# Kernel tuning notes

Measured on AMD Instinct MI355X. Metric: run time of the kernel, lower is better.

## Reference

```python
import jax, jax.numpy as jnp
import numpy as np

N, E, D, HGC, LG, NC = 20000, 320000, 256, 256, 4, 2
BN_EPS = 1e-5


def setup_inputs() -> dict:
    key = jax.random.key(0)
    ks = jax.random.split(key, 12)
    features = jax.random.normal(ks[0], (N, D), jnp.float32)
    edge_index = jax.random.randint(ks[1], (2, E), 0, N)
    edgenet_input = jax.random.uniform(ks[2], (E, 6), dtype=jnp.float32)
    edge_weight_override = jax.random.uniform(ks[3], (E,), dtype=jnp.float32)
    # ChebConv weights: K=3 weight matrices per layer; layer0 in=D==HGC so one stack works
    cheb_w = jax.random.normal(ks[4], (LG, 3, HGC, HGC), jnp.float32) * np.float32((2.0 / HGC) ** 0.5)
    w1 = jax.random.normal(ks[5], (LG * HGC, 256), jnp.float32) * np.float32((2.0 / (LG * HGC)) ** 0.5)
    b1 = jnp.zeros((256,), jnp.float32)
    bn_gamma = jnp.ones((256,), jnp.float32)
    bn_beta = jnp.zeros((256,), jnp.float32)
    bn_mean = jnp.zeros((256,), jnp.float32)
    bn_var = jnp.ones((256,), jnp.float32)
    w2 = jax.random.normal(ks[6], (256, NC), jnp.float32) * np.float32((2.0 / 256.0) ** 0.5)
    b2 = jnp.zeros((NC,), jnp.float32)
    return dict(features=features, edge_index=edge_index, edgenet_input=edgenet_input,
                edge_weight_override=edge_weight_override, cheb_w=cheb_w,
                w1=w1, b1=b1, bn_gamma=bn_gamma, bn_beta=bn_beta,
                bn_mean=bn_mean, bn_var=bn_var, w2=w2, b2=b2)


def reference(features, edge_index, edgenet_input, edge_weight_override, cheb_w,
              w1, b1, bn_gamma, bn_beta, bn_mean, bn_var, w2, b2):
    # eval mode: dropout / edge_dropout are no-ops; edge_weight_override bypasses PAE
    ew = edge_weight_override  # [E]
    row, col = edge_index[0], edge_index[1]  # source, target (PyG source_to_target)
    n = features.shape[0]
    # sym-normalized scaled Laplacian, lambda_max=2: L_hat = -D^{-1/2} A D^{-1/2} (diag 1-1=0)
    deg = jax.ops.segment_sum(ew, row, num_segments=n)
    dis = jnp.where(deg > 0, jax.lax.rsqrt(deg), 0.0)
    norm = -(dis[row] * ew * dis[col])  # [E]

    def prop(x):  # out[col] += norm * x[row]
        return jax.ops.segment_sum(norm[:, None] * x[row], col, num_segments=n)

    def cheb(x, W):  # W: [3, in, out]; Chebyshev recursion T0=x, T1=L_hat x, T2=2 L_hat T1 - T0
        tx0 = x
        tx1 = prop(x)
        out = tx0 @ W[0] + tx1 @ W[1]
        tx2 = 2.0 * prop(tx1) - tx0
        return out + tx2 @ W[2]

    h = jax.nn.relu(cheb(features, cheb_w[0]))
    jk = h
    for i in range(1, cheb_w.shape[0]):
        h = jax.nn.relu(cheb(h, cheb_w[i]))
        jk = jnp.concatenate((jk, h), axis=1)
    # classifier: Linear -> ReLU -> BatchNorm1d(eval) -> Linear
    z = jax.nn.relu(jk @ w1 + b1)
    z = (z - bn_mean) * (bn_gamma * jax.lax.rsqrt(bn_var + BN_EPS)) + bn_beta
    logit = z @ w2 + b2
    return logit, ew
```

## Files before the change

### kernel.cpp

```cpp
#include <hip/hip_runtime.h>
#include <hip/hip_bf16.h>

#define NN 20000
#define EE 320000
#define LGN 4

typedef unsigned short u16;
typedef short bf16x8 __attribute__((ext_vector_type(8)));
typedef float f32x4 __attribute__((ext_vector_type(4)));

__device__ __forceinline__ float bf2f(u16 v) {
    unsigned int u = ((unsigned int)v) << 16;
    float f; __builtin_memcpy(&f, &u, 4); return f;
}
__device__ __forceinline__ u16 f2bf(float f) {
    __hip_bfloat16 h = __float2bfloat16(f);
    u16 u; __builtin_memcpy(&u, &h, 2); return u;
}

__device__ __forceinline__ void gll16(const void* g, void* l) {
    __builtin_amdgcn_global_load_lds(
        (const __attribute__((address_space(1))) unsigned int*)g,
        (__attribute__((address_space(3))) unsigned int*)l, 16, 0, 0);
}

__global__ __launch_bounds__(256) void k_edge1(const int* __restrict__ ei,
                                               const float* __restrict__ ew,
                                               float* __restrict__ deg,
                                               int* __restrict__ counts,
                                               float* __restrict__ out_ew) {
    int e = blockIdx.x * 256 + threadIdx.x;
    if (e >= EE) return;
    int r = ei[e];
    float w = ew[e];
    atomicAdd(&deg[r], w);
    atomicAdd(&counts[ei[EE + e]], 1);
    out_ew[e] = w;
}

__global__ __launch_bounds__(256) void k_rsqrt(float* __restrict__ deg) {
    int i = blockIdx.x * 256 + threadIdx.x;
    if (i >= NN) return;
    float d = deg[i];
    deg[i] = (d > 0.f) ? rsqrtf(d) : 0.f;
}

__global__ __launch_bounds__(1024) void k_scan(const int* __restrict__ counts,
                                               int* __restrict__ offs) {
    __shared__ int part[1024];
    int t = threadIdx.x;
    const int C = (NN + 1023) / 1024;
    int lo = t * C, hi = min(lo + C, NN);
    int s = 0;
    for (int i = lo; i < hi; i++) s += counts[i];
    part[t] = s;
    __syncthreads();
    for (int off = 1; off < 1024; off <<= 1) {
        int add = (t >= off) ? part[t - off] : 0;
        __syncthreads();
        part[t] += add;
        __syncthreads();
    }
    int base = part[t] - s;
    for (int i = lo; i < hi; i++) { offs[i] = base; base += counts[i]; }
    if (t == 1023) offs[NN] = part[1023];
}

__global__ __launch_bounds__(256) void k_scatter(const int* __restrict__ ei,
                                                 const float* __restrict__ ew,
                                                 const float* __restrict__ dis,
                                                 const int* __restrict__ offs,
                                                 int* __restrict__ cursor,
                                                 int2* __restrict__ nbrs) {
    int e = blockIdx.x * 256 + threadIdx.x;
    if (e >= EE) return;
    int r = ei[e], c = ei[EE + e];
    float nm = -(dis[r] * ew[e] * dis[c]);
    int pidx = offs[c] + atomicAdd(&cursor[c], 1);
    nbrs[pidx] = make_int2(r, __float_as_int(nm));
}

__global__ __launch_bounds__(256) void k_cast(const float* __restrict__ src,
                                              u16* __restrict__ dst, int n) {
    int i = blockIdx.x * 256 + threadIdx.x;
    if (i < n) dst[i] = f2bf(src[i]);
}

__global__ __launch_bounds__(256) void k_cast_T(const float* __restrict__ src,
                                                u16* __restrict__ dst, int K) {
    __shared__ u16 tile[32][33];
    int kt = blockIdx.x * 32, nt = blockIdx.y * 32;
    int tx = threadIdx.x & 31, ty = threadIdx.x >> 5;
#pragma unroll
    for (int i = 0; i < 32; i += 8)
        tile[ty + i][tx] = f2bf(src[(size_t)(kt + ty + i) * 256 + (nt + tx)]);
    __syncthreads();
#pragma unroll
    for (int i = 0; i < 32; i += 8)
        dst[(size_t)(nt + ty + i) * K + (kt + tx)] = tile[tx][ty + i];
}

__global__ __launch_bounds__(256) void k_foldbn(const float* __restrict__ g,
                                                const float* __restrict__ be,
                                                const float* __restrict__ mn,
                                                const float* __restrict__ vr,
                                                float* __restrict__ sc,
                                                float* __restrict__ sh) {
    int t = threadIdx.x;
    if (t < 256) {
        float s = g[t] * rsqrtf(vr[t] + 1e-5f);
        sc[t] = s;
        sh[t] = be[t] - mn[t] * s;
    }
}

__global__ __launch_bounds__(256) void k_prop(const u16* __restrict__ x, int ldx,
                                              const u16* __restrict__ xsub, int ldsub,
                                              int dotx2,
                                              u16* __restrict__ out, int ldo,
                                              const int* __restrict__ offs,
                                              const int2* __restrict__ nbrs) {
    int c = __builtin_amdgcn_readfirstlane(blockIdx.x * 4 + (threadIdx.x >> 6));
    int lane = threadIdx.x & 63;
    int s = offs[c], e = offs[c + 1];
    float a0 = 0.f, a1 = 0.f, a2 = 0.f, a3 = 0.f;
    for (int i = s; i < e; i += 8) {
        int2 mm[8];
        ushort4 xv[8];
#pragma unroll
        for (int j = 0; j < 8; j++) mm[j] = nbrs[i + j];
#pragma unroll
        for (int j = 0; j < 8; j++)
            xv[j] = *(const ushort4*)(x + (size_t)mm[j].x * ldx + lane * 4);
#pragma unroll
        for (int j = 0; j < 8; j++) {
            float w = (i + j < e) ? __int_as_float(mm[j].y) : 0.f;
            a0 += w * bf2f(xv[j].x);
            a1 += w * bf2f(xv[j].y);
            a2 += w * bf2f(xv[j].z);
            a3 += w * bf2f(xv[j].w);
        }
    }
    if (dotx2) {
        ushort4 xs = *(const ushort4*)(xsub + (size_t)c * ldsub + lane * 4);
        a0 = 2.f * a0 - bf2f(xs.x);
        a1 = 2.f * a1 - bf2f(xs.y);
        a2 = 2.f * a2 - bf2f(xs.z);
        a3 = 2.f * a3 - bf2f(xs.w);
    }
    ushort4 o;
    o.x = f2bf(a0); o.y = f2bf(a1); o.z = f2bf(a2); o.w = f2bf(a3);
    *(ushort4*)(out + (size_t)c * ldo + lane * 4) = o;
}

__global__ __launch_bounds__(256, 2) void k_gemm(
    const u16* __restrict__ A0, const u16* __restrict__ A1,
    const u16* __restrict__ A2, const u16* __restrict__ A3,
    int lda0, int lda1, int lda2, int lda3,
    int K, const u16* __restrict__ Bt,
    int mode,
    u16* __restrict__ outb, int ldob,
    const float* __restrict__ bias, const float* __restrict__ sc,
    const float* __restrict__ sh,
    const float* __restrict__ w2, const float* __restrict__ b2,
    float* __restrict__ outlog) {
    __shared__ __align__(16) u16 lds[2 * 20 * 512];
    int t = threadIdx.x;
    int wv = t >> 6, l = t & 63;
    int q = l >> 4, l16 = l & 15;
    int m0 = blockIdx.x * 64;
    int n0 = wv * 64;
    const int steps = K >> 5;

    f32x4 acc[4][4] = {};

    int arow = min(m0 + wv * 16 + l16, NN - 1);

    auto stage = [&](int buf, int s) {
        int kt = s * 32;
        u16* base = lds + buf * 20 * 512;
#pragma unroll
        for (int j = 0; j < 4; j++) {
            const u16* bg = Bt + (size_t)((wv * 4 + j) * 16 + l16) * K + kt + q * 8;
            gll16(bg, base + (wv * 4 + j) * 512);
        }
        int ch = kt >> 8;
        const u16* ap;
        int la;
        if (ch == 0) { ap = A0; la = lda0; }
        else if (ch == 1) { ap = A1; la = lda1; }
        else if (ch == 2) { ap = A2; la = lda2; }
        else { ap = A3; la = lda3; }
        gll16(ap + (size_t)arow * la + (kt & 255) + q * 8, base + (16 + wv) * 512);
    };

    stage(0, 0);
    for (int s = 0; s < steps; s++) {
        __syncthreads();
        if (s + 1 < steps) stage((s + 1) & 1, s + 1);
        const u16* base = lds + (s & 1) * 20 * 512;
        bf16x8 a[4], b[4];
#pragma unroll
        for (int mh = 0; mh < 4; mh++)
            a[mh] = *(const bf16x8*)(base + (16 + mh) * 512 + l * 8);
#pragma unroll
        for (int j = 0; j < 4; j++)
            b[j] = *(const bf16x8*)(base + (wv * 4 + j) * 512 + l * 8);
#pragma unroll
        for (int mh = 0; mh < 4; mh++)
#pragma unroll
            for (int j = 0; j < 4; j++)
                acc[mh][j] =
                    __builtin_amdgcn_mfma_f32_16x16x32_bf16(a[mh], b[j], acc[mh][j], 0, 0, 0);
    }
    __syncthreads();

    if (mode == 0) {
        u16* Cs = lds + wv * 4608;
#pragma unroll
        for (int mh = 0; mh < 4; mh++)
#pragma unroll
            for (int j = 0; j < 4; j++)
#pragma unroll
                for (int i = 0; i < 4; i++) {
                    float v = acc[mh][j][i];
                    v = v > 0.f ? v : 0.f;
                    Cs[(mh * 16 + q * 4 + i) * 72 + j * 16 + l16] = f2bf(v);
                }
#pragma unroll
        for (int j = 0; j < 8; j++) {
            int f = j * 64 + l;
            int r = f >> 3, cc = (f & 7) * 8;
            uint4 cv = *(const uint4*)&Cs[r * 72 + cc];
            int row = m0 + r;
            if (row < NN) *(uint4*)(outb + (size_t)row * ldob + n0 + cc) = cv;
        }
    } else {
        float bi[4], s4[4], h4[4], wa[4], wb[4];
#pragma unroll
        for (int j = 0; j < 4; j++) {
            int col = n0 + j * 16 + l16;
            bi[j] = bias[col];
            s4[j] = sc[col];
            h4[j] = sh[col];
            wa[j] = w2[2 * col];
            wb[j] = w2[2 * col + 1];
        }
        float* red = (float*)lds;
#pragma unroll
        for (int mh = 0; mh < 4; mh++)
#pragma unroll
            for (int i = 0; i < 4; i++) {
                float p0 = 0.f, p1 = 0.f;
#pragma unroll
                for (int j = 0; j < 4; j++) {
                    float v = acc[mh][j][i] + bi[j];
                    v = v > 0.f ? v : 0.f;
                    v = v * s4[j] + h4[j];
                    p0 += v * wa[j];
                    p1 += v * wb[j];
                }
#pragma unroll
                for (int off = 1; off < 16; off <<= 1) {
                    p0 += __shfl_xor(p0, off, 64);
                    p1 += __shfl_xor(p1, off, 64);
                }
                if (l16 == 0) {
                    int rl = mh * 16 + q * 4 + i;
                    red[(wv * 64 + rl) * 2 + 0] = p0;
                    red[(wv * 64 + rl) * 2 + 1] = p1;
                }
            }
        __syncthreads();
        if (t < 128) {
            int rl = t >> 1, cp = t & 1;
            float v = red[(0 * 64 + rl) * 2 + cp] + red[(1 * 64 + rl) * 2 + cp] +
                      red[(2 * 64 + rl) * 2 + cp] + red[(3 * 64 + rl) * 2 + cp];
            int row = m0 + rl;
            if (row < NN) outlog[(size_t)row * 2 + cp] = v + b2[cp];
        }
    }
}

extern "C" void kernel_launch(void* const* d_in, const int* in_sizes, int n_in,
                              void* d_out, int out_size, void* d_ws, size_t ws_size,
                              hipStream_t stream) {
    const float* features = (const float*)d_in[0];
    const int* ei = (const int*)d_in[1];
    const float* ew = (const float*)d_in[3];
    const float* cheb_w = (const float*)d_in[4];
    const float* w1 = (const float*)d_in[5];
    const float* b1 = (const float*)d_in[6];
    const float* g = (const float*)d_in[7];
    const float* be = (const float*)d_in[8];
    const float* mn = (const float*)d_in[9];
    const float* vr = (const float*)d_in[10];
    const float* w2 = (const float*)d_in[11];
    const float* b2 = (const float*)d_in[12];
    float* out = (float*)d_out;

    char* p = (char*)d_ws;
    auto alloc = [&](size_t bytes) -> char* {
        char* r = p;
        p += (bytes + 255) & ~(size_t)255;
        return r;
    };
    float* deg = (float*)alloc((size_t)NN * 4);
    int* counts = (int*)alloc((size_t)(NN + 1) * 4);
    int* cursor = (int*)alloc((size_t)NN * 4);
    size_t zero_bytes = (size_t)(p - (char*)deg);
    int* offs = (int*)alloc((size_t)(NN + 1) * 4);
    int2* nbrs = (int2*)alloc((size_t)(EE + 8) * 8);
    u16* xb = (u16*)alloc((size_t)NN * 256 * 2);
    u16* tx1 = (u16*)alloc((size_t)NN * 256 * 2);
    u16* tx2 = (u16*)alloc((size_t)NN * 256 * 2);
    u16* jk = (u16*)alloc((size_t)NN * 1024 * 2);
    u16* chebT = (u16*)alloc((size_t)LGN * 3 * 256 * 256 * 2);
    u16* w1T = (u16*)alloc((size_t)1024 * 256 * 2);
    float* sc = (float*)alloc(256 * 4);
    float* sh = (float*)alloc(256 * 4);

    hipMemsetAsync(deg, 0, zero_bytes, stream);
    hipMemsetAsync(nbrs + EE, 0, 8 * sizeof(int2), stream);
    k_edge1<<<(EE + 255) / 256, 256, 0, stream>>>(ei, ew, deg, counts, out + (size_t)NN * 2);
    k_rsqrt<<<(NN + 255) / 256, 256, 0, stream>>>(deg);
    k_scan<<<1, 1024, 0, stream>>>(counts, offs);
    k_scatter<<<(EE + 255) / 256, 256, 0, stream>>>(ei, ew, deg, offs, cursor, nbrs);
    k_cast<<<((NN * 256) + 255) / 256, 256, 0, stream>>>(features, xb, NN * 256);
    for (int i = 0; i < LGN; i++)
        k_cast_T<<<dim3(24, 8), 256, 0, stream>>>(cheb_w + (size_t)i * 768 * 256,
                                                  chebT + (size_t)i * 256 * 768, 768);
    k_cast_T<<<dim3(32, 8), 256, 0, stream>>>(w1, w1T, 1024);
    k_foldbn<<<1, 256, 0, stream>>>(g, be, mn, vr, sc, sh);

    const int gg = (NN + 63) / 64;
    for (int i = 0; i < LGN; i++) {
        const u16* x = (i == 0) ? xb : (jk + (size_t)(i - 1) * 256);
        int ldx = (i == 0) ? 256 : 1024;
        k_prop<<<NN / 4, 256, 0, stream>>>(x, ldx, (const u16*)nullptr, 0, 0, tx1, 256, offs,
                                           nbrs);
        k_prop<<<NN / 4, 256, 0, stream>>>(tx1, 256, x, ldx, 1, tx2, 256, offs, nbrs);
        k_gemm<<<gg, 256, 0, stream>>>(
            x, tx1, tx2, (const u16*)nullptr, ldx, 256, 256, 0, 768,
            chebT + (size_t)i * 256 * 768, 0, jk + (size_t)i * 256, 1024, (const float*)nullptr,
            (const float*)nullptr, (const float*)nullptr, (const float*)nullptr,
            (const float*)nullptr, (float*)nullptr);
    }
    k_gemm<<<gg, 256, 0, stream>>>(jk, jk + 256, jk + 512, jk + 768, 1024, 1024, 1024, 1024,
                                   1024, w1T, 1, (u16*)nullptr, 0, b1, sc, sh, w2, b2, out);
}
```

Before: 526.9 us.

## Widen gather loads in prop, drop LDS staging in GEMM, fuse rsqrt

The propagation kernel now has each half-wave handle alternate neighbors with 16-byte row loads, processes 16 neighbors per iteration, and combines the two halves with a cross-lane shuffle. The GEMM drops its double-buffered LDS staging and reads A rows and B fragments straight from global memory into MFMA operands. B is pre-packed into fragment order by a new cast kernel, and launch bounds move to 3 blocks per CU. The rsqrt kernel is folded into the scatter kernel and the per-layer weight casts become a single launch. Direct global loads in the GEMM lose LDS reuse and may raise memory traffic, in exchange for fewer barriers and higher occupancy.

```diff
diff --git a/kernel.cpp b/kernel.cpp
--- a/kernel.cpp
+++ b/kernel.cpp
@@ -7,6 +7,7 @@
 
 typedef unsigned short u16;
 typedef short bf16x8 __attribute__((ext_vector_type(8)));
+typedef unsigned short u16x8 __attribute__((ext_vector_type(8)));
 typedef float f32x4 __attribute__((ext_vector_type(4)));
 
 __device__ __forceinline__ float bf2f(u16 v) {
@@ -16,12 +17,6 @@
 __device__ __forceinline__ u16 f2bf(float f) {
     __hip_bfloat16 h = __float2bfloat16(f);
     u16 u; __builtin_memcpy(&u, &h, 2); return u;
-}
-
-__device__ __forceinline__ void gll16(const void* g, void* l) {
-    __builtin_amdgcn_global_load_lds(
-        (const __attribute__((address_space(1))) unsigned int*)g,
-        (__attribute__((address_space(3))) unsigned int*)l, 16, 0, 0);
 }
 
 __global__ __launch_bounds__(256) void k_edge1(const int* __restrict__ ei,
@@ -36,13 +31,6 @@
     atomicAdd(&deg[r], w);
     atomicAdd(&counts[ei[EE + e]], 1);
     out_ew[e] = w;
-}
-
-__global__ __launch_bounds__(256) void k_rsqrt(float* __restrict__ deg) {
-    int i = blockIdx.x * 256 + threadIdx.x;
-    if (i >= NN) return;
-    float d = deg[i];
-    deg[i] = (d > 0.f) ? rsqrtf(d) : 0.f;
 }
 
 __global__ __launch_bounds__(1024) void k_scan(const int* __restrict__ counts,
@@ -68,14 +56,17 @@
 
 __global__ __launch_bounds__(256) void k_scatter(const int* __restrict__ ei,
                                                  const float* __restrict__ ew,
-                                                 const float* __restrict__ dis,
+                                                 const float* __restrict__ deg,
                                                  const int* __restrict__ offs,
                                                  int* __restrict__ cursor,
                                                  int2* __restrict__ nbrs) {
     int e = blockIdx.x * 256 + threadIdx.x;
     if (e >= EE) return;
     int r = ei[e], c = ei[EE + e];
-    float nm = -(dis[r] * ew[e] * dis[c]);
+    float dr = deg[r], dc = deg[c];
+    float ir = (dr > 0.f) ? rsqrtf(dr) : 0.f;
+    float ic = (dc > 0.f) ? rsqrtf(dc) : 0.f;
+    float nm = -(ir * ew[e] * ic);
     int pidx = offs[c] + atomicAdd(&cursor[c], 1);
     nbrs[pidx] = make_int2(r, __float_as_int(nm));
 }
@@ -86,18 +77,19 @@
     if (i < n) dst[i] = f2bf(src[i]);
 }
 
-__global__ __launch_bounds__(256) void k_cast_T(const float* __restrict__ src,
-                                                u16* __restrict__ dst, int K) {
-    __shared__ u16 tile[32][33];
-    int kt = blockIdx.x * 32, nt = blockIdx.y * 32;
-    int tx = threadIdx.x & 31, ty = threadIdx.x >> 5;
-#pragma unroll
-    for (int i = 0; i < 32; i += 8)
-        tile[ty + i][tx] = f2bf(src[(size_t)(kt + ty + i) * 256 + (nt + tx)]);
-    __syncthreads();
-#pragma unroll
-    for (int i = 0; i < 32; i += 8)
-        dst[(size_t)(nt + ty + i) * K + (kt + tx)] = tile[tx][ty + i];
+__global__ __launch_bounds__(256) void k_castB(const float* __restrict__ src,
+                                               u16* __restrict__ dst, int K) {
+    src += (size_t)blockIdx.y * K * 256;
+    dst += (size_t)blockIdx.y * K * 256;
+    int tid = blockIdx.x * 256 + threadIdx.x;
+    if (tid >= (K >> 5) * 1024) return;
+    int l = tid & 63, f = (tid >> 6) & 15, s = tid >> 10;
+    int col = f * 16 + (l & 15);
+    int kb = s * 32 + ((l >> 4) << 3);
+    u16 tmp[8];
+#pragma unroll
+    for (int j = 0; j < 8; j++) tmp[j] = f2bf(src[(size_t)(kb + j) * 256 + col]);
+    *(uint4*)(dst + (size_t)tid * 8) = *(uint4*)tmp;
 }
 
 __global__ __launch_bounds__(256) void k_foldbn(const float* __restrict__ g,
@@ -121,99 +113,147 @@
                                               const int* __restrict__ offs,
                                               const int2* __restrict__ nbrs) {
     int c = __builtin_amdgcn_readfirstlane(blockIdx.x * 4 + (threadIdx.x >> 6));
-    int lane = threadIdx.x & 63;
+    int l = threadIdx.x & 63;
+    int hf = l >> 5;
+    int cl = l & 31;
     int s = offs[c], e = offs[c + 1];
-    float a0 = 0.f, a1 = 0.f, a2 = 0.f, a3 = 0.f;
-    for (int i = s; i < e; i += 8) {
+    float acc0 = 0.f, acc1 = 0.f, acc2 = 0.f, acc3 = 0.f;
+    float acc4 = 0.f, acc5 = 0.f, acc6 = 0.f, acc7 = 0.f;
+    for (int i = s; i < e; i += 16) {
         int2 mm[8];
-        ushort4 xv[8];
-#pragma unroll
-        for (int j = 0; j < 8; j++) mm[j] = nbrs[i + j];
-#pragma unroll
-        for (int j = 0; j < 8; j++)
-            xv[j] = *(const ushort4*)(x + (size_t)mm[j].x * ldx + lane * 4);
-#pragma unroll
-        for (int j = 0; j < 8; j++) {
-            float w = (i + j < e) ? __int_as_float(mm[j].y) : 0.f;
-            a0 += w * bf2f(xv[j].x);
-            a1 += w * bf2f(xv[j].y);
-            a2 += w * bf2f(xv[j].z);
-            a3 += w * bf2f(xv[j].w);
-        }
-    }
+        u16x8 xv[8];
+#pragma unroll
+        for (int j = 0; j < 4; j++) mm[j] = nbrs[i + 2 * j + hf];
+#pragma unroll
+        for (int j = 0; j < 4; j++)
+            xv[j] = *(const u16x8*)(x + (size_t)mm[j].x * ldx + cl * 8);
+        bool more = (i + 8 < e);
+        if (more) {
+#pragma unroll
+            for (int j = 4; j < 8; j++) mm[j] = nbrs[i + 2 * j + hf];
+#pragma unroll
+            for (int j = 4; j < 8; j++)
+                xv[j] = *(const u16x8*)(x + (size_t)mm[j].x * ldx + cl * 8);
+        }
+#pragma unroll
+        for (int j = 0; j < 4; j++) {
+            float w = (i + 2 * j + hf < e) ? __int_as_float(mm[j].y) : 0.f;
+            acc0 += w * bf2f(xv[j][0]);
+            acc1 += w * bf2f(xv[j][1]);
+            acc2 += w * bf2f(xv[j][2]);
+            acc3 += w * bf2f(xv[j][3]);
+            acc4 += w * bf2f(xv[j][4]);
+            acc5 += w * bf2f(xv[j][5]);
+            acc6 += w * bf2f(xv[j][6]);
+            acc7 += w * bf2f(xv[j][7]);
+        }
+        if (more) {
+#pragma unroll
+            for (int j = 4; j < 8; j++) {
+                float w = (i + 2 * j + hf < e) ? __int_as_float(mm[j].y) : 0.f;
+                acc0 += w * bf2f(xv[j][0]);
+                acc1 += w * bf2f(xv[j][1]);
+                acc2 += w * bf2f(xv[j][2]);
+                acc3 += w * bf2f(xv[j][3]);
+                acc4 += w * bf2f(xv[j][4]);
+                acc5 += w * bf2f(xv[j][5]);
+                acc6 += w * bf2f(xv[j][6]);
+                acc7 += w * bf2f(xv[j][7]);
+            }
+        }
+    }
+    acc0 += __shfl_xor(acc0, 32, 64);
+    acc1 += __shfl_xor(acc1, 32, 64);
+    acc2 += __shfl_xor(acc2, 32, 64);
+    acc3 += __shfl_xor(acc3, 32, 64);
+    acc4 += __shfl_xor(acc4, 32, 64);
+    acc5 += __shfl_xor(acc5, 32, 64);
+    acc6 += __shfl_xor(acc6, 32, 64);
+    acc7 += __shfl_xor(acc7, 32, 64);
     if (dotx2) {
-        ushort4 xs = *(const ushort4*)(xsub + (size_t)c * ldsub + lane * 4);
-        a0 = 2.f * a0 - bf2f(xs.x);
-        a1 = 2.f * a1 - bf2f(xs.y);
-        a2 = 2.f * a2 - bf2f(xs.z);
-        a3 = 2.f * a3 - bf2f(xs.w);
-    }
-    ushort4 o;
-    o.x = f2bf(a0); o.y = f2bf(a1); o.z = f2bf(a2); o.w = f2bf(a3);
-    *(ushort4*)(out + (size_t)c * ldo + lane * 4) = o;
-}
-
-__global__ __launch_bounds__(256, 2) void k_gemm(
+        u16x8 xs = *(const u16x8*)(xsub + (size_t)c * ldsub + cl * 8);
+        acc0 = 2.f * acc0 - bf2f(xs[0]);
+        acc1 = 2.f * acc1 - bf2f(xs[1]);
+        acc2 = 2.f * acc2 - bf2f(xs[2]);
+        acc3 = 2.f * acc3 - bf2f(xs[3]);
+        acc4 = 2.f * acc4 - bf2f(xs[4]);
+        acc5 = 2.f * acc5 - bf2f(xs[5]);
+        acc6 = 2.f * acc6 - bf2f(xs[6]);
+        acc7 = 2.f * acc7 - bf2f(xs[7]);
+    }
+    if (hf == 0) {
+        u16 o[8];
+        o[0] = f2bf(acc0); o[1] = f2bf(acc1); o[2] = f2bf(acc2); o[3] = f2bf(acc3);
+        o[4] = f2bf(acc4); o[5] = f2bf(acc5); o[6] = f2bf(acc6); o[7] = f2bf(acc7);
+        *(uint4*)(out + (size_t)c * ldo + cl * 8) = *(uint4*)o;
+    }
+}
+
+__global__ __launch_bounds__(256, 3) void k_gemm(
     const u16* __restrict__ A0, const u16* __restrict__ A1,
     const u16* __restrict__ A2, const u16* __restrict__ A3,
     int lda0, int lda1, int lda2, int lda3,
-    int K, const u16* __restrict__ Bt,
+    int K, const u16* __restrict__ Bf,
     int mode,
     u16* __restrict__ outb, int ldob,
     const float* __restrict__ bias, const float* __restrict__ sc,
     const float* __restrict__ sh,
     const float* __restrict__ w2, const float* __restrict__ b2,
     float* __restrict__ outlog) {
-    __shared__ __align__(16) u16 lds[2 * 20 * 512];
+    __shared__ __align__(16) u16 lds[18432];
     int t = threadIdx.x;
     int wv = t >> 6, l = t & 63;
     int q = l >> 4, l16 = l & 15;
     int m0 = blockIdx.x * 64;
     int n0 = wv * 64;
-    const int steps = K >> 5;
 
     f32x4 acc[4][4] = {};
 
-    int arow = min(m0 + wv * 16 + l16, NN - 1);
-
-    auto stage = [&](int buf, int s) {
-        int kt = s * 32;
-        u16* base = lds + buf * 20 * 512;
-#pragma unroll
-        for (int j = 0; j < 4; j++) {
-            const u16* bg = Bt + (size_t)((wv * 4 + j) * 16 + l16) * K + kt + q * 8;
-            gll16(bg, base + (wv * 4 + j) * 512);
-        }
-        int ch = kt >> 8;
-        const u16* ap;
-        int la;
+    int rmh[4];
+#pragma unroll
+    for (int mh = 0; mh < 4; mh++) rmh[mh] = min(m0 + mh * 16 + l16, NN - 1);
+
+    const u16* bfw = Bf + (size_t)(wv * 4) * 512 + (size_t)l * 8;
+    const int nch = K >> 8;
+    for (int ch = 0; ch < nch; ch++) {
+        const u16* ap; int la;
         if (ch == 0) { ap = A0; la = lda0; }
         else if (ch == 1) { ap = A1; la = lda1; }
         else if (ch == 2) { ap = A2; la = lda2; }
         else { ap = A3; la = lda3; }
-        gll16(ap + (size_t)arow * la + (kt & 255) + q * 8, base + (16 + wv) * 512);
-    };
-
-    stage(0, 0);
-    for (int s = 0; s < steps; s++) {
-        __syncthreads();
-        if (s + 1 < steps) stage((s + 1) & 1, s + 1);
-        const u16* base = lds + (s & 1) * 20 * 512;
-        bf16x8 a[4], b[4];
-#pragma unroll
-        for (int mh = 0; mh < 4; mh++)
-            a[mh] = *(const bf16x8*)(base + (16 + mh) * 512 + l * 8);
-#pragma unroll
-        for (int j = 0; j < 4; j++)
-            b[j] = *(const bf16x8*)(base + (wv * 4 + j) * 512 + l * 8);
-#pragma unroll
-        for (int mh = 0; mh < 4; mh++)
-#pragma unroll
-            for (int j = 0; j < 4; j++)
-                acc[mh][j] =
-                    __builtin_amdgcn_mfma_f32_16x16x32_bf16(a[mh], b[j], acc[mh][j], 0, 0, 0);
-    }
-    __syncthreads();
+        const u16* aw0 = ap + (size_t)rmh[0] * la + q * 8;
+        const u16* aw1 = ap + (size_t)rmh[1] * la + q * 8;
+        const u16* aw2 = ap + (size_t)rmh[2] * la + q * 8;
+        const u16* aw3 = ap + (size_t)rmh[3] * la + q * 8;
+        const u16* bch = bfw + (size_t)ch * 8 * 8192;
+#pragma unroll
+        for (int ss = 0; ss < 8; ss++) {
+            bf16x8 a0 = *(const bf16x8*)(aw0 + ss * 32);
+            bf16x8 a1 = *(const bf16x8*)(aw1 + ss * 32);
+            bf16x8 a2 = *(const bf16x8*)(aw2 + ss * 32);
+            bf16x8 a3 = *(const bf16x8*)(aw3 + ss * 32);
+            bf16x8 b0 = *(const bf16x8*)(bch + ss * 8192 + 0 * 512);
+            bf16x8 b1 = *(const bf16x8*)(bch + ss * 8192 + 1 * 512);
+            bf16x8 b2v = *(const bf16x8*)(bch + ss * 8192 + 2 * 512);
+            bf16x8 b3 = *(const bf16x8*)(bch + ss * 8192 + 3 * 512);
+            acc[0][0] = __builtin_amdgcn_mfma_f32_16x16x32_bf16(a0, b0, acc[0][0], 0, 0, 0);
+            acc[0][1] = __builtin_amdgcn_mfma_f32_16x16x32_bf16(a0, b1, acc[0][1], 0, 0, 0);
+            acc[0][2] = __builtin_amdgcn_mfma_f32_16x16x32_bf16(a0, b2v, acc[0][2], 0, 0, 0);
+            acc[0][3] = __builtin_amdgcn_mfma_f32_16x16x32_bf16(a0, b3, acc[0][3], 0, 0, 0);
+            acc[1][0] = __builtin_amdgcn_mfma_f32_16x16x32_bf16(a1, b0, acc[1][0], 0, 0, 0);
+            acc[1][1] = __builtin_amdgcn_mfma_f32_16x16x32_bf16(a1, b1, acc[1][1], 0, 0, 0);
+            acc[1][2] = __builtin_amdgcn_mfma_f32_16x16x32_bf16(a1, b2v, acc[1][2], 0, 0, 0);
+            acc[1][3] = __builtin_amdgcn_mfma_f32_16x16x32_bf16(a1, b3, acc[1][3], 0, 0, 0);
+            acc[2][0] = __builtin_amdgcn_mfma_f32_16x16x32_bf16(a2, b0, acc[2][0], 0, 0, 0);
+            acc[2][1] = __builtin_amdgcn_mfma_f32_16x16x32_bf16(a2, b1, acc[2][1], 0, 0, 0);
+            acc[2][2] = __builtin_amdgcn_mfma_f32_16x16x32_bf16(a2, b2v, acc[2][2], 0, 0, 0);
+            acc[2][3] = __builtin_amdgcn_mfma_f32_16x16x32_bf16(a2, b3, acc[2][3], 0, 0, 0);
+            acc[3][0] = __builtin_amdgcn_mfma_f32_16x16x32_bf16(a3, b0, acc[3][0], 0, 0, 0);
+            acc[3][1] = __builtin_amdgcn_mfma_f32_16x16x32_bf16(a3, b1, acc[3][1], 0, 0, 0);
+            acc[3][2] = __builtin_amdgcn_mfma_f32_16x16x32_bf16(a3, b2v, acc[3][2], 0, 0, 0);
+            acc[3][3] = __builtin_amdgcn_mfma_f32_16x16x32_bf16(a3, b3, acc[3][3], 0, 0, 0);
+        }
+    }
 
     if (mode == 0) {
         u16* Cs = lds + wv * 4608;
@@ -310,7 +350,7 @@
     int* cursor = (int*)alloc((size_t)NN * 4);
     size_t zero_bytes = (size_t)(p - (char*)deg);
     int* offs = (int*)alloc((size_t)(NN + 1) * 4);
-    int2* nbrs = (int2*)alloc((size_t)(EE + 8) * 8);
+    int2* nbrs = (int2*)alloc((size_t)(EE + 16) * 8);
     u16* xb = (u16*)alloc((size_t)NN * 256 * 2);
     u16* tx1 = (u16*)alloc((size_t)NN * 256 * 2);
     u16* tx2 = (u16*)alloc((size_t)NN * 256 * 2);
@@ -321,16 +361,13 @@
     float* sh = (float*)alloc(256 * 4);
 
     hipMemsetAsync(deg, 0, zero_bytes, stream);
-    hipMemsetAsync(nbrs + EE, 0, 8 * sizeof(int2), stream);
+    hipMemsetAsync(nbrs + EE, 0, 16 * sizeof(int2), stream);
     k_edge1<<<(EE + 255) / 256, 256, 0, stream>>>(ei, ew, deg, counts, out + (size_t)NN * 2);
-    k_rsqrt<<<(NN + 255) / 256, 256, 0, stream>>>(deg);
     k_scan<<<1, 1024, 0, stream>>>(counts, offs);
     k_scatter<<<(EE + 255) / 256, 256, 0, stream>>>(ei, ew, deg, offs, cursor, nbrs);
     k_cast<<<((NN * 256) + 255) / 256, 256, 0, stream>>>(features, xb, NN * 256);
-    for (int i = 0; i < LGN; i++)
-        k_cast_T<<<dim3(24, 8), 256, 0, stream>>>(cheb_w + (size_t)i * 768 * 256,
-                                                  chebT + (size_t)i * 256 * 768, 768);
-    k_cast_T<<<dim3(32, 8), 256, 0, stream>>>(w1, w1T, 1024);
+    k_castB<<<dim3(96, LGN), 256, 0, stream>>>(cheb_w, chebT, 768);
+    k_castB<<<dim3(128, 1), 256, 0, stream>>>(w1, w1T, 1024);
     k_foldbn<<<1, 256, 0, stream>>>(g, be, mn, vr, sc, sh);
 
     const int gg = (NN + 63) / 64;
```

Result: no change. 529.2 us (+0.4%).
